# Performance work log

Hardware: AMD Instinct MI355X
Metric: run time of the kernel (lower is better)

## Reference

```python
import jax, jax.numpy as jnp
import numpy as np

ATTEN_SIZE = 16
HIDDEN = 512


def setup_inputs() -> dict:
    key = jax.random.key(0)
    ks = jax.random.split(key, 6)
    B, S, D_in, H, D_out = 64, 100, 256, HIDDEN, 256
    # xavier-normal-ish scale for weights
    def xav(k, shape):
        fan_in, fan_out = shape
        std = np.sqrt(2.0 / (fan_in + fan_out))
        return jax.random.normal(k, shape, dtype=jnp.float32) * std
    return {
        "x": jax.random.normal(ks[0], (B, S, D_in), dtype=jnp.float32),
        "W0": xav(ks[1], (D_in, H)),
        "b0": jnp.zeros((1, 1, H), dtype=jnp.float32),
        "Wq": xav(ks[2], (H, H)),
        "Wk": xav(ks[3], (H, H)),
        "Wv": xav(ks[4], (H, H)),
        "W1": xav(ks[5], (H, D_out)),
        "b1": jnp.zeros((1, 1, D_out), dtype=jnp.float32),
    }


def reference(x, W0, b0, Wq, Wk, Wv, W1, b1):
    w = ATTEN_SIZE
    win = 2 * w + 1
    B, S = x.shape[0], x.shape[1]
    # pre-attention MLP layer (atten_layer_index = 1)
    h = jax.nn.relu(x @ W0 + b0)  # [B, S, H]
    # sliding-window neighbor gather, matching pad + roll(k) + stack + slice:
    # x_nei[:, i, k_idx] = padded[:, i + 2w - k_idx]  (reversed window order)
    padded = jnp.pad(h, ((0, 0), (w, w), (0, 0)))  # [B, S+2w, H]
    idx = jnp.arange(S)[:, None] + (2 * w - jnp.arange(win))[None, :]
    x_nei = padded[:, idx]
    q = x_nei @ Wq
    k = x_nei @ Wk
    v = x_nei @ Wv
    d = jnp.einsum('bswh,buh_->bswu'.replace('h_', 'sh'[1] + 'h'), q, k) if False else jnp.einsum('bswh,bsuh->bswu', q, k)
    d = d / jnp.sqrt(jnp.float32(HIDDEN))
    alpha = jax.nn.softmax(d, axis=-1)
    wv = jnp.einsum('bswu,bsuh->bswh', alpha, v)
    out = wv.sum(axis=2)  # sum over window rows -> [B, S, H]
    y = jax.nn.relu(out @ W1 + b1)  # [B, S, D_out]
    return y, alpha.reshape(B * S, win, win)
```

## Files before the change

kernel.cpp:

```cpp
#include <hip/hip_runtime.h>

typedef __bf16 bf16x8 __attribute__((ext_vector_type(8)));
typedef float f32x4 __attribute__((ext_vector_type(4)));
typedef unsigned int u32;

__device__ __forceinline__ unsigned short f2bf(float f) {
  unsigned int u = __float_as_uint(f);
  u += 0x7FFFu + ((u >> 16) & 1u);
  return (unsigned short)(u >> 16);
}

__device__ __forceinline__ void gload16(const void* g, void* l) {
  __builtin_amdgcn_global_load_lds(
      (const __attribute__((address_space(1))) u32*)g,
      (__attribute__((address_space(3))) u32*)l, 16, 0, 0);
}

__global__ __launch_bounds__(256) void prep_kernel(
    const float* __restrict__ x, const float* __restrict__ W0,
    const float* __restrict__ Wq, const float* __restrict__ Wk,
    const float* __restrict__ Wv, const float* __restrict__ W1,
    unsigned short* __restrict__ xb, unsigned short* __restrict__ w0t,
    unsigned short* __restrict__ wqkvt, unsigned short* __restrict__ w1t)
{
  __shared__ float tile[32][33];
  const int bid = blockIdx.x, tid = threadIdx.x;
  if (bid < 1600) {
    long i = (long)bid * 1024 + tid * 4;
    float4 v = *(const float4*)(x + i);
    ushort4 o = {f2bf(v.x), f2bf(v.y), f2bf(v.z), f2bf(v.w)};
    *(ushort4*)(xb + i) = o;
    return;
  }
  int id = bid - 1600;
  const float* src; unsigned short* dst;
  int N, DLD, k0, n0, drow0;
  if (id < 128) {
    src = W0; N = 512; dst = w0t; DLD = 256;
    k0 = (id >> 4) * 32; n0 = (id & 15) * 32; drow0 = n0;
  } else if (id < 896) {
    int id1 = id - 128, which = id1 >> 8, rem = id1 & 255;
    src = (which == 0) ? Wq : (which == 1) ? Wk : Wv;
    N = 512; dst = wqkvt; DLD = 512;
    k0 = (rem >> 4) * 32; n0 = (rem & 15) * 32; drow0 = which * 512 + n0;
  } else {
    int id2 = id - 896;
    src = W1; N = 256; dst = w1t; DLD = 512;
    k0 = (id2 >> 3) * 32; n0 = (id2 & 7) * 32; drow0 = n0;
  }
  const int tr = tid >> 5, tc = tid & 31;
#pragma unroll
  for (int rr = 0; rr < 4; ++rr) {
    int kl = tr + rr * 8;
    tile[kl][tc] = src[(long)(k0 + kl) * N + n0 + tc];
  }
  __syncthreads();
#pragma unroll
  for (int rr = 0; rr < 4; ++rr) {
    int nl = tr + rr * 8;
    dst[(long)(drow0 + nl) * DLD + k0 + tc] = f2bf(tile[tc][nl]);
  }
}

template<bool RELU, bool OUT_BF16>
__global__ __launch_bounds__(256) void gemm_tile(
    const unsigned short* __restrict__ A, int lda,
    const unsigned short* __restrict__ Bt, int ldb,
    const float* __restrict__ bias,
    void* __restrict__ Cout, int ldc, int KT)
{
  __shared__ unsigned short As[2][64 * 32];
  __shared__ unsigned short Bs[2][128 * 32];
  const int tid = threadIdx.x;
  const int m0 = blockIdx.x * 64;
  const int n0 = blockIdx.y * 128;
  const int w = tid >> 6, lane = tid & 63;
  const int lr = lane & 15, kq = lane >> 4;
  const int cg  = (tid & 3) ^ ((tid >> 3) & 3);
  const int kqs = kq ^ ((lr >> 1) & 3);

  const unsigned short* Ag  = A  + (long)(m0 + (tid >> 2)) * lda + cg * 8;
  const unsigned short* Bg0 = Bt + (long)(n0 + (tid >> 2)) * ldb + cg * 8;
  const unsigned short* Bg1 = Bg0 + (long)64 * ldb;

  f32x4 acc[4][2];
#pragma unroll
  for (int i = 0; i < 4; i++)
#pragma unroll
    for (int j = 0; j < 2; j++) acc[i][j] = (f32x4){0.f, 0.f, 0.f, 0.f};

#define STAGE(buf, kt) do { int ko = (kt) * 32;                      \
    gload16(Ag + ko,  &As[buf][tid * 8]);                            \
    gload16(Bg0 + ko, &Bs[buf][tid * 8]);                            \
    gload16(Bg1 + ko, &Bs[buf][(tid + 256) * 8]); } while (0)

  STAGE(0, 0);
  __syncthreads();
  int cur = 0;
  for (int kt = 0; kt < KT; ++kt) {
    if (kt + 1 < KT) STAGE(cur ^ 1, kt + 1);
    bf16x8 af[4], bfr[2];
#pragma unroll
    for (int ii = 0; ii < 4; ii++)
      af[ii] = *(const bf16x8*)&As[cur][(16 * ii + lr) * 32 + 8 * kqs];
#pragma unroll
    for (int jj = 0; jj < 2; jj++)
      bfr[jj] = *(const bf16x8*)&Bs[cur][(w * 32 + 16 * jj + lr) * 32 + 8 * kqs];
#pragma unroll
    for (int ii = 0; ii < 4; ii++)
#pragma unroll
      for (int jj = 0; jj < 2; jj++)
        acc[ii][jj] = __builtin_amdgcn_mfma_f32_16x16x32_bf16(af[ii], bfr[jj], acc[ii][jj], 0, 0, 0);
    __syncthreads();
    cur ^= 1;
  }
#undef STAGE

#pragma unroll
  for (int ii = 0; ii < 4; ii++) {
#pragma unroll
    for (int jj = 0; jj < 2; jj++) {
      int col = n0 + w * 32 + 16 * jj + lr;
      float bv = bias ? bias[col] : 0.0f;
#pragma unroll
      for (int r = 0; r < 4; r++) {
        int row = m0 + 16 * ii + 4 * kq + r;
        float v = acc[ii][jj][r] + bv;
        if (RELU) v = fmaxf(v, 0.0f);
        if (OUT_BF16) ((unsigned short*)Cout)[(long)row * ldc + col] = f2bf(v);
        else          ((float*)Cout)[(long)row * ldc + col] = v;
      }
    }
  }
}

__global__ __launch_bounds__(256) void gram_tile(
    const unsigned short* __restrict__ qkv, float* __restrict__ G)
{
  const float scale = 0.044194173824159216f;
  __shared__ unsigned short As[2][64 * 32];
  __shared__ unsigned short Bs[2][64 * 32];
  const int tid = threadIdx.x;
  const int m0 = (blockIdx.x & 1) * 64;
  const int n0 = (blockIdx.x >> 1) * 64;
  const int b  = blockIdx.y;
  const int w = tid >> 6, lane = tid & 63;
  const int lr = lane & 15, kq = lane >> 4;
  const int cg  = (tid & 3) ^ ((tid >> 3) & 3);
  const int kqs = kq ^ ((lr >> 1) & 3);

  const unsigned short* A  = qkv + (long)b * 100 * 1536;
  const unsigned short* Bt = A + 512;
  const unsigned short* Ag = A  + (long)(m0 + (tid >> 2)) * 1536 + cg * 8;
  const unsigned short* Bg = Bt + (long)(n0 + (tid >> 2)) * 1536 + cg * 8;

  f32x4 acc[4];
#pragma unroll
  for (int i = 0; i < 4; i++) acc[i] = (f32x4){0.f, 0.f, 0.f, 0.f};

#define STAGEG(buf, kt) do { int ko = (kt) * 32;                     \
    gload16(Ag + ko, &As[buf][tid * 8]);                             \
    gload16(Bg + ko, &Bs[buf][tid * 8]); } while (0)

  STAGEG(0, 0);
  __syncthreads();
  int cur = 0;
  for (int kt = 0; kt < 16; ++kt) {
    if (kt + 1 < 16) STAGEG(cur ^ 1, kt + 1);
    bf16x8 bk = *(const bf16x8*)&Bs[cur][(16 * w + lr) * 32 + 8 * kqs];
    bf16x8 af[4];
#pragma unroll
    for (int ii = 0; ii < 4; ii++)
      af[ii] = *(const bf16x8*)&As[cur][(16 * ii + lr) * 32 + 8 * kqs];
#pragma unroll
    for (int ii = 0; ii < 4; ii++)
      acc[ii] = __builtin_amdgcn_mfma_f32_16x16x32_bf16(af[ii], bk, acc[ii], 0, 0, 0);
    __syncthreads();
    cur ^= 1;
  }
#undef STAGEG

  float* Gb = G + (long)b * 10000;
  int j = n0 + w * 16 + lr;
#pragma unroll
  for (int ii = 0; ii < 4; ii++) {
#pragma unroll
    for (int r = 0; r < 4; r++) {
      int i = m0 + 16 * ii + 4 * kq + r;
      if (i < 100 && j < 100) Gb[i * 100 + j] = acc[ii][r] * scale;
    }
  }
}

__global__ __launch_bounds__(256) void attn_kernel(
    const float* __restrict__ G,
    const unsigned short* __restrict__ qkv,
    float* __restrict__ alpha_out,
    unsigned short* __restrict__ outb)
{
  const int blk = blockIdx.x;
  const int b = blk / 100, s = blk % 100;
  __shared__ float E[33][36];
  __shared__ float rinv[33];
  __shared__ float beta[36];
  const int tid = threadIdx.x;
  const float* Gb = G + (long)b * 10000;

  for (int t = tid; t < 1089; t += 256) {
    int dw = t / 33, du = t % 33;
    int i = s + 16 - dw, j = s + 16 - du;
    float v = 0.f;
    if ((unsigned)i < 100u && (unsigned)j < 100u) v = Gb[i * 100 + j];
    E[dw][du] = __expf(v);
  }
  __syncthreads();

  if (tid < 132) {
    int row = tid >> 2, g = tid & 3;
    float ssum = 0.f;
    for (int u = g; u < 33; u += 4) ssum += E[row][u];
    ssum += __shfl_xor(ssum, 1);
    ssum += __shfl_xor(ssum, 2);
    if (g == 0) rinv[row] = 1.0f / ssum;
  }
  __syncthreads();

  float* aout = alpha_out + (long)blk * 1089;
  for (int t = tid; t < 1089; t += 256) {
    int dw = t / 33, du = t % 33;
    aout[t] = E[dw][du] * rinv[dw];
  }
  if (tid < 132) {
    int col = tid >> 2, g = tid & 3;
    float sum = 0.f;
    for (int w = g; w < 33; w += 4) sum += E[w][col] * rinv[w];
    sum += __shfl_xor(sum, 1);
    sum += __shfl_xor(sum, 2);
    if (g == 0) beta[col] = sum;
  }
  __syncthreads();

  const unsigned short* vbase = qkv + (long)(b * 100) * 1536 + 1024;
  {
    float acc0 = 0.f, acc1 = 0.f;
    for (int u = 0; u < 33; ++u) {
      int p = s + 16 - u;
      if ((unsigned)p < 100u) {
        float bw = beta[u];
        u32 pv = *(const u32*)(vbase + (long)p * 1536 + 2 * tid);
        acc0 = fmaf(bw, __uint_as_float(pv << 16), acc0);
        acc1 = fmaf(bw, __uint_as_float(pv & 0xFFFF0000u), acc1);
      }
    }
    u32 packed = (u32)f2bf(acc0) | ((u32)f2bf(acc1) << 16);
    *(u32*)(outb + (long)blk * 512 + 2 * tid) = packed;
  }
}

extern "C" void kernel_launch(void* const* d_in, const int* in_sizes, int n_in,
                              void* d_out, int out_size, void* d_ws, size_t ws_size,
                              hipStream_t stream) {
  const float* x  = (const float*)d_in[0];
  const float* W0 = (const float*)d_in[1];
  const float* b0 = (const float*)d_in[2];
  const float* Wq = (const float*)d_in[3];
  const float* Wk = (const float*)d_in[4];
  const float* Wv = (const float*)d_in[5];
  const float* W1 = (const float*)d_in[6];
  const float* b1 = (const float*)d_in[7];

  char* ws = (char*)d_ws;
  unsigned short* xb    = (unsigned short*)(ws + 0);
  unsigned short* w0t   = (unsigned short*)(ws + 3276800);
  unsigned short* wqkvt = (unsigned short*)(ws + 3538944);
  unsigned short* w1t   = (unsigned short*)(ws + 5111808);
  unsigned short* h     = (unsigned short*)(ws + 5373952);
  unsigned short* qkv   = (unsigned short*)(ws + 11927552);
  float*          G     = (float*)(ws + 31686656);
  unsigned short* outb  = (unsigned short*)(ws + 34246656);

  float* y_out     = (float*)d_out;
  float* alpha_out = y_out + 6400 * 256;

  prep_kernel<<<2624, 256, 0, stream>>>(x, W0, Wq, Wk, Wv, W1, xb, w0t, wqkvt, w1t);
  gemm_tile<true,  true ><<<dim3(100, 4),  256, 0, stream>>>(xb, 256, w0t, 256, b0, h, 512, 8);
  gemm_tile<false, true ><<<dim3(100, 12), 256, 0, stream>>>(h, 512, wqkvt, 512, nullptr, qkv, 1536, 16);
  gram_tile<<<dim3(4, 64), 256, 0, stream>>>(qkv, G);
  attn_kernel<<<6400, 256, 0, stream>>>(G, qkv, alpha_out, outb);
  gemm_tile<true,  false><<<dim3(100, 2),  256, 0, stream>>>(outb, 512, w1t, 512, b1, y_out, 256, 16);
}
```

Measured before the change: 174.8 us.

## Process four sequence positions per attention block to reuse V loads

The attention kernel now handles four consecutive positions per block, so the grid shrinks from one block per position to one per four positions. Each block loads 36 V rows once and accumulates into four outputs, instead of each position reloading its 33 overlapping V rows. It also gives better thread utilisation in the softmax reductions. The cost is a shared-memory footprint about four times larger and fewer blocks, which lowers occupancy and parallelism.

```diff
diff --git a/kernel.cpp b/kernel.cpp
--- a/kernel.cpp
+++ b/kernel.cpp
@@ -192,68 +192,80 @@
   }
 }
 
-__global__ __launch_bounds__(256) void attn_kernel(
+__global__ __launch_bounds__(256) void attn_kernel4(
     const float* __restrict__ G,
     const unsigned short* __restrict__ qkv,
     float* __restrict__ alpha_out,
     unsigned short* __restrict__ outb)
 {
   const int blk = blockIdx.x;
-  const int b = blk / 100, s = blk % 100;
-  __shared__ float E[33][36];
-  __shared__ float rinv[33];
-  __shared__ float beta[36];
+  const int b = blk / 25, s0 = (blk % 25) * 4;
+  __shared__ float E[4][33][36];
+  __shared__ float rinv[4][33];
+  __shared__ float beta[4][36];
   const int tid = threadIdx.x;
   const float* Gb = G + (long)b * 10000;
 
-  for (int t = tid; t < 1089; t += 256) {
-    int dw = t / 33, du = t % 33;
+  for (int t = tid; t < 4356; t += 256) {
+    int si = t / 1089, r = t - si * 1089;
+    int dw = r / 33, du = r - dw * 33;
+    int s = s0 + si;
     int i = s + 16 - dw, j = s + 16 - du;
     float v = 0.f;
     if ((unsigned)i < 100u && (unsigned)j < 100u) v = Gb[i * 100 + j];
-    E[dw][du] = __expf(v);
-  }
-  __syncthreads();
-
-  if (tid < 132) {
-    int row = tid >> 2, g = tid & 3;
+    E[si][dw][du] = __expf(v);
+  }
+  __syncthreads();
+
+  for (int t = tid; t < 528; t += 256) {
+    int q = t >> 2, g = t & 3;
+    int si = q / 33, row = q - si * 33;
     float ssum = 0.f;
-    for (int u = g; u < 33; u += 4) ssum += E[row][u];
+    for (int u = g; u < 33; u += 4) ssum += E[si][row][u];
     ssum += __shfl_xor(ssum, 1);
     ssum += __shfl_xor(ssum, 2);
-    if (g == 0) rinv[row] = 1.0f / ssum;
-  }
-  __syncthreads();
-
-  float* aout = alpha_out + (long)blk * 1089;
-  for (int t = tid; t < 1089; t += 256) {
-    int dw = t / 33, du = t % 33;
-    aout[t] = E[dw][du] * rinv[dw];
-  }
-  if (tid < 132) {
-    int col = tid >> 2, g = tid & 3;
+    if (g == 0) rinv[si][row] = 1.0f / ssum;
+  }
+  __syncthreads();
+
+  for (int t = tid; t < 4356; t += 256) {
+    int si = t / 1089, r = t - si * 1089;
+    int dw = r / 33;
+    alpha_out[(long)(b * 100 + s0 + si) * 1089 + r] = E[si][dw][r - dw * 33] * rinv[si][dw];
+  }
+  for (int t = tid; t < 528; t += 256) {
+    int q = t >> 2, g = t & 3;
+    int si = q / 33, col = q - si * 33;
     float sum = 0.f;
-    for (int w = g; w < 33; w += 4) sum += E[w][col] * rinv[w];
+    for (int w = g; w < 33; w += 4) sum += E[si][w][col] * rinv[si][w];
     sum += __shfl_xor(sum, 1);
     sum += __shfl_xor(sum, 2);
-    if (g == 0) beta[col] = sum;
+    if (g == 0) beta[si][col] = sum;
   }
   __syncthreads();
 
   const unsigned short* vbase = qkv + (long)(b * 100) * 1536 + 1024;
-  {
-    float acc0 = 0.f, acc1 = 0.f;
-    for (int u = 0; u < 33; ++u) {
-      int p = s + 16 - u;
-      if ((unsigned)p < 100u) {
-        float bw = beta[u];
-        u32 pv = *(const u32*)(vbase + (long)p * 1536 + 2 * tid);
-        acc0 = fmaf(bw, __uint_as_float(pv << 16), acc0);
-        acc1 = fmaf(bw, __uint_as_float(pv & 0xFFFF0000u), acc1);
+  float a0[4] = {0.f, 0.f, 0.f, 0.f}, a1[4] = {0.f, 0.f, 0.f, 0.f};
+  for (int p = s0 - 16; p < s0 + 20; ++p) {
+    if ((unsigned)p < 100u) {
+      u32 pv = *(const u32*)(vbase + (long)p * 1536 + 2 * tid);
+      float v0 = __uint_as_float(pv << 16);
+      float v1 = __uint_as_float(pv & 0xFFFF0000u);
+#pragma unroll
+      for (int si = 0; si < 4; ++si) {
+        int u = s0 + si + 16 - p;
+        if ((unsigned)u < 33u) {
+          float bw = beta[si][u];
+          a0[si] = fmaf(bw, v0, a0[si]);
+          a1[si] = fmaf(bw, v1, a1[si]);
+        }
       }
     }
-    u32 packed = (u32)f2bf(acc0) | ((u32)f2bf(acc1) << 16);
-    *(u32*)(outb + (long)blk * 512 + 2 * tid) = packed;
+  }
+#pragma unroll
+  for (int si = 0; si < 4; ++si) {
+    u32 packed = (u32)f2bf(a0[si]) | ((u32)f2bf(a1[si]) << 16);
+    *(u32*)(outb + (long)(b * 100 + s0 + si) * 512 + 2 * tid) = packed;
   }
 }
 
@@ -286,6 +298,6 @@
   gemm_tile<true,  true ><<<dim3(100, 4),  256, 0, stream>>>(xb, 256, w0t, 256, b0, h, 512, 8);
   gemm_tile<false, true ><<<dim3(100, 12), 256, 0, stream>>>(h, 512, wqkvt, 512, nullptr, qkv, 1536, 16);
   gram_tile<<<dim3(4, 64), 256, 0, stream>>>(qkv, G);
-  attn_kernel<<<6400, 256, 0, stream>>>(G, qkv, alpha_out, outb);
+  attn_kernel4<<<1600, 256, 0, stream>>>(G, qkv, alpha_out, outb);
   gemm_tile<true,  false><<<dim3(100, 2),  256, 0, stream>>>(outb, 512, w1t, 512, b1, y_out, 256, 16);
 }
```

New measurement: 172.8 us. About the same (-1.1%).
